# Optimization experiments

Measured on AMD Instinct MI355X. Metric: run time of the kernel, lower is better.

Reference implementation:

```python
import jax, jax.numpy as jnp
import numpy as np

N_QUBITS = 4
N_LAYERS = 2
BATCH = 262144


def _bc(theta, ndim):
    # broadcast per-sample angles [B] against a state slice of given ndim
    t = jnp.asarray(theta)
    if t.ndim == 1:
        t = t.reshape((-1,) + (1,) * (ndim - 1))
    return t


def _apply_ry(state, wire, theta):
    # RY(t) = [[cos(t/2), -sin(t/2)], [sin(t/2), cos(t/2)]]
    a0 = jax.lax.index_in_dim(state, 0, axis=wire + 1, keepdims=False)
    a1 = jax.lax.index_in_dim(state, 1, axis=wire + 1, keepdims=False)
    t = _bc(theta, a0.ndim) * 0.5
    c = jnp.cos(t).astype(state.dtype)
    s = jnp.sin(t).astype(state.dtype)
    return jnp.stack([c * a0 - s * a1, s * a0 + c * a1], axis=wire + 1)


def _apply_rz(state, wire, theta):
    # RZ(t) = diag(exp(-i t/2), exp(+i t/2))
    a0 = jax.lax.index_in_dim(state, 0, axis=wire + 1, keepdims=False)
    a1 = jax.lax.index_in_dim(state, 1, axis=wire + 1, keepdims=False)
    t = _bc(theta, a0.ndim) * 0.5
    p = (jnp.cos(t) - 1j * jnp.sin(t)).astype(state.dtype)  # exp(-i t/2)
    return jnp.stack([p * a0, jnp.conj(p) * a1], axis=wire + 1)


def _cnot(state, control, target):
    s0 = jax.lax.index_in_dim(state, 0, axis=control + 1, keepdims=False)
    s1 = jax.lax.index_in_dim(state, 1, axis=control + 1, keepdims=False)
    # axis of target wire after removing the control axis (batch is axis 0)
    t_ax = target + 1 if target < control else target
    s1 = jnp.flip(s1, axis=t_ax)
    return jnp.stack([s0, s1], axis=control + 1)


def setup_inputs() -> dict:
    key = jax.random.key(0)
    kx, kw = jax.random.split(key)
    x = jax.random.uniform(kx, (BATCH, N_QUBITS), dtype=jnp.float32)
    weights = 0.1 * jax.random.normal(kw, (N_LAYERS, N_QUBITS, 2), dtype=jnp.float32)
    return {"x": x, "weights": weights}


def reference(x, weights):
    B = x.shape[0]
    # |0...0> for every sample: [B, 2, 2, 2, 2] complex64
    state = jnp.zeros((B,) + (2,) * N_QUBITS, dtype=jnp.complex64)
    state = state.at[(slice(None),) + (0,) * N_QUBITS].set(1.0)
    # data encoding: per-sample RY on each wire
    for i in range(N_QUBITS):
        state = _apply_ry(state, i, x[:, i])
    # variational layers (shared angles across the batch)
    for layer in range(N_LAYERS):
        for i in range(N_QUBITS):
            state = _apply_ry(state, i, weights[layer, i, 0])
            state = _apply_rz(state, i, weights[layer, i, 1])
        for i in range(N_QUBITS - 1):
            state = _cnot(state, i, i + 1)
        state = _cnot(state, N_QUBITS - 1, 0)
    # <Z_0> = P(bit0=0) - P(bit0=1)
    probs = (state.real ** 2 + state.imag ** 2).reshape(B, 2, -1)
    expz = jnp.sum(probs[:, 0], axis=-1) - jnp.sum(probs[:, 1], axis=-1)
    return expz[:, None].astype(jnp.float32)
```

## Files before the change

kernel.cpp:

```cpp
#include <hip/hip_runtime.h>
#include <math.h>


__global__ __launch_bounds__(256) void qc_main(const float* __restrict__ x,
                                               const float* __restrict__ w,
                                               float* __restrict__ out, int B) {
    int b = blockIdx.x * blockDim.x + threadIdx.x;
    if (b >= B) return;

    float4 xv = reinterpret_cast<const float4*>(x)[b];
    float xs[4] = {xv.x, xv.y, xv.z, xv.w};

    float fr[4][2], fi[4][2];
#pragma unroll
    for (int q = 0; q < 4; ++q) {
        float Cq, Sq, gr, gi;
        __sincosf(0.5f * (xs[q] + w[2 * q]), &Sq, &Cq);
        __sincosf(w[2 * q + 1], &gi, &gr);
        fr[q][0] = Cq;       fi[q][0] = 0.0f;
        fr[q][1] = Sq * gr;  fi[q][1] = Sq * gi;
    }

    float t01r[4], t01i[4], t23r[4], t23i[4];
#pragma unroll
    for (int p = 0; p < 4; ++p) {
        const int hb = p >> 1, lb = p & 1;
        t01r[p] = fr[0][hb] * fr[1][lb] - fi[0][hb] * fi[1][lb];
        t01i[p] = fr[0][hb] * fi[1][lb] + fi[0][hb] * fr[1][lb];
        t23r[p] = fr[2][hb] * fr[3][lb] - fi[2][hb] * fi[3][lb];
        t23i[p] = fr[2][hb] * fi[3][lb] + fi[2][hb] * fr[3][lb];
    }
    float ar[16], ai[16];
#pragma unroll
    for (int idx = 0; idx < 16; ++idx) {
        const int p = idx >> 2, r = idx & 3;
        ar[idx] = t01r[p] * t23r[r] - t01i[p] * t23i[r];
        ai[idx] = t01r[p] * t23i[r] + t01i[p] * t23r[r];
    }

#pragma unroll
    for (int k = 0; k < 4; ++k) {
        const int cm = 8 >> k, tm = 8 >> ((k + 1) & 3);
#pragma unroll
        for (int idx = 0; idx < 16; ++idx) {
            if ((idx & cm) && !(idx & tm)) {
                const int j = idx | tm;
                float tr = ar[idx]; ar[idx] = ar[j]; ar[j] = tr;
                float ti = ai[idx]; ai[idx] = ai[j]; ai[j] = ti;
            }
        }
    }

    float zr[16], zi[16];
#pragma unroll
    for (int idx = 0; idx < 16; ++idx) { zr[idx] = ar[idx]; zi[idx] = ai[idx]; }
#pragma unroll
    for (int q = 1; q < 4; ++q) {
        float sa, ca;
        __sincosf(w[8 + 2 * q], &sa, &ca);
        const int m = 8 >> q;
#pragma unroll
        for (int idx = 0; idx < 16; ++idx) {
            if ((idx & m) == 0) {
                const int i1 = idx | m;
                float v0r = zr[idx], v0i = zi[idx];
                float v1r = zr[i1], v1i = zi[i1];
                zr[idx] = ca * v0r - sa * v1r;
                zi[idx] = ca * v0i - sa * v1i;
                zr[i1] = -sa * v0r - ca * v1r;
                zi[i1] = -sa * v0i - ca * v1i;
            }
        }
    }

    float e = 0.0f;
#pragma unroll
    for (int idx = 0; idx < 16; ++idx) e += ar[idx] * zr[idx] + ai[idx] * zi[idx];
    out[b] = e;
}

extern "C" void kernel_launch(void* const* d_in, const int* in_sizes, int n_in,
                              void* d_out, int out_size, void* d_ws, size_t ws_size,
                              hipStream_t stream) {
    const float* x = (const float*)d_in[0];
    const float* w = (const float*)d_in[1];
    float* out = (float*)d_out;
    const int B = in_sizes[0] / 4;
    const int threads = 256;
    const int blocks = (B + threads - 1) / threads;
    qc_main<<<blocks, threads, 0, stream>>>(x, w, out, B);
}
```

Before: 57.57 us.

## Replace state-vector simulation with closed-form expectation polynomial

Derives a closed-form trigonometric polynomial for <Z0> in terms of per-sample angle sines and cosines, with weight-only coefficients K1..K8 computed once per thread. This removes the 16-amplitude complex state construction, the CNOT permutations and the observable application, cutting per-thread ALU and register use. The kernel was likely already memory-bound at this size, so the gain may be limited. Correctness relies on the derived coefficient algebra being exact.

```diff
diff --git a/kernel.cpp b/kernel.cpp
--- a/kernel.cpp
+++ b/kernel.cpp
@@ -9,73 +9,38 @@
     if (b >= B) return;
 
     float4 xv = reinterpret_cast<const float4*>(x)[b];
-    float xs[4] = {xv.x, xv.y, xv.z, xv.w};
 
-    float fr[4][2], fi[4][2];
+    float CB[4], SB[4];
 #pragma unroll
-    for (int q = 0; q < 4; ++q) {
-        float Cq, Sq, gr, gi;
-        __sincosf(0.5f * (xs[q] + w[2 * q]), &Sq, &Cq);
-        __sincosf(w[2 * q + 1], &gi, &gr);
-        fr[q][0] = Cq;       fi[q][0] = 0.0f;
-        fr[q][1] = Sq * gr;  fi[q][1] = Sq * gi;
-    }
+    for (int q = 0; q < 4; ++q) __sincosf(w[2 * q + 1], &SB[q], &CB[q]);
+    float c[4], s[4];
+#pragma unroll
+    for (int q = 1; q < 4; ++q) __sincosf(w[8 + 2 * q], &s[q], &c[q]);
 
-    float t01r[4], t01i[4], t23r[4], t23i[4];
-#pragma unroll
-    for (int p = 0; p < 4; ++p) {
-        const int hb = p >> 1, lb = p & 1;
-        t01r[p] = fr[0][hb] * fr[1][lb] - fi[0][hb] * fi[1][lb];
-        t01i[p] = fr[0][hb] * fi[1][lb] + fi[0][hb] * fr[1][lb];
-        t23r[p] = fr[2][hb] * fr[3][lb] - fi[2][hb] * fi[3][lb];
-        t23i[p] = fr[2][hb] * fi[3][lb] + fi[2][hb] * fr[3][lb];
-    }
-    float ar[16], ai[16];
-#pragma unroll
-    for (int idx = 0; idx < 16; ++idx) {
-        const int p = idx >> 2, r = idx & 3;
-        ar[idx] = t01r[p] * t23r[r] - t01i[p] * t23i[r];
-        ai[idx] = t01r[p] * t23i[r] + t01i[p] * t23r[r];
-    }
+    const float K1 =  c[1] * c[2] * c[3];
+    const float K2 = -c[1] * c[2] * s[3] * CB[0] * CB[1] * CB[3];
+    const float K3 =  c[1] * s[2] * c[3] * SB[2] * SB[3];
+    const float K4 = -c[1] * s[2] * s[3] * SB[0] * SB[1] * CB[2];
+    const float K5 = -s[1] * c[2] * c[3] * CB[1] * CB[2];
+    const float K6 = -s[1] * c[2] * s[3] * SB[0] * SB[2] * CB[3];
+    const float K7 = -s[1] * s[2] * c[3] * SB[1] * SB[3];
+    const float K8 = -s[1] * s[2] * s[3] * CB[0];
 
-#pragma unroll
-    for (int k = 0; k < 4; ++k) {
-        const int cm = 8 >> k, tm = 8 >> ((k + 1) & 3);
-#pragma unroll
-        for (int idx = 0; idx < 16; ++idx) {
-            if ((idx & cm) && !(idx & tm)) {
-                const int j = idx | tm;
-                float tr = ar[idx]; ar[idx] = ar[j]; ar[j] = tr;
-                float ti = ai[idx]; ai[idx] = ai[j]; ai[j] = ti;
-            }
-        }
-    }
+    float S0, C0, S1, C1, S2, C2, S3, C3;
+    __sincosf(xv.x + w[0], &S0, &C0);
+    __sincosf(xv.y + w[2], &S1, &C1);
+    __sincosf(xv.z + w[4], &S2, &C2);
+    __sincosf(xv.w + w[6], &S3, &C3);
 
-    float zr[16], zi[16];
-#pragma unroll
-    for (int idx = 0; idx < 16; ++idx) { zr[idx] = ar[idx]; zi[idx] = ai[idx]; }
-#pragma unroll
-    for (int q = 1; q < 4; ++q) {
-        float sa, ca;
-        __sincosf(w[8 + 2 * q], &sa, &ca);
-        const int m = 8 >> q;
-#pragma unroll
-        for (int idx = 0; idx < 16; ++idx) {
-            if ((idx & m) == 0) {
-                const int i1 = idx | m;
-                float v0r = zr[idx], v0i = zi[idx];
-                float v1r = zr[i1], v1i = zi[i1];
-                zr[idx] = ca * v0r - sa * v1r;
-                zi[idx] = ca * v0i - sa * v1i;
-                zr[i1] = -sa * v0r - ca * v1r;
-                zi[i1] = -sa * v0i - ca * v1i;
-            }
-        }
-    }
-
-    float e = 0.0f;
-#pragma unroll
-    for (int idx = 0; idx < 16; ++idx) e += ar[idx] * zr[idx] + ai[idx] * zi[idx];
+    const float p01 = S0 * S1, p23 = S2 * S3, c2s3 = C2 * S3;
+    float e = K1 * (C0 * C1 * C3);
+    e = fmaf(K2, p01 * c2s3, e);
+    e = fmaf(K3, p23, e);
+    e = fmaf(K4, p01 * S2, e);
+    e = fmaf(K5, S1 * S2 * C3, e);
+    e = fmaf(K6, S0 * C1 * p23, e);
+    e = fmaf(K7, C0 * S1 * c2s3, e);
+    e = fmaf(K8, S0, e);
     out[b] = e;
 }
 
```

Measured after the change: 55.51 us. 3.6% less time.
